# Kernel tuning notes

Hardware: AMD Instinct MI355X
Metric: run time of the kernel (lower is better)

## Reference

```python
import jax, jax.numpy as jnp
from jax import lax
import numpy as np

B, C, T = 8, 1024, 4096
H, K = 16, 7
PAD_L, PAD_R = 6, 0  # causal padding = kernel_size - 1
STRIDE = 1


def setup_inputs() -> dict:
    key = jax.random.key(0)
    k1, k2 = jax.random.split(key)
    x = jax.random.normal(k1, (B, C, T), dtype=jnp.float32)
    # xavier_uniform for [H, 1, K]: bound = sqrt(6 / (fan_in + fan_out)) with fan_in=K, fan_out=H*K? torch uses fan_in=1*K, fan_out=H*K/ groups... use simple uniform scale ~ sqrt(6/(1*K + 1*K))
    bound = float(np.sqrt(6.0 / (K + K)))
    weight = jax.random.uniform(k2, (H, 1, K), dtype=jnp.float32, minval=-bound, maxval=bound)
    bias = jnp.zeros((H,), dtype=jnp.float32)
    return {"x": x, "weight": weight, "bias": bias}


def reference(x, weight, bias):
    """Lightweight convolution: softmax-normalized shared-weight depthwise conv1d.
    x: [B, C, T]; weight: [H, 1, K]; bias: [H].
    """
    b, c, t = x.shape
    h = weight.shape[0]
    n = c // h  # channels per head sharing one kernel
    w = jax.nn.softmax(weight, axis=-1)  # [H, 1, K]
    # fold the shared-channel groups into the batch dim: [B*N, H, T]
    xr = x.reshape(b * n, h, t)
    xp = jnp.pad(xr, ((0, 0), (0, 0), (PAD_L, PAD_R)))
    out = lax.conv_general_dilated(
        xp, w,
        window_strides=(STRIDE,),
        padding='VALID',
        dimension_numbers=('NCH', 'OIH', 'NCH'),
        feature_group_count=h,
    )  # [B*N, H, T]
    out = out + bias[None, :, None]
    return out.reshape(b, c, t)
```

## Files before the change

kernel.cpp:

```cpp
#include <hip/hip_runtime.h>
#include <math.h>

#define TT 4096
#define KK 7
#define HH 16

__global__ void softmax_w_kernel(const float* __restrict__ w,
                                 float* __restrict__ wsm) {
    int h = threadIdx.x;
    if (h < HH) {
        float v[KK];
        float m = -1e30f;
        #pragma unroll
        for (int k = 0; k < KK; ++k) { v[k] = w[h * KK + k]; m = fmaxf(m, v[k]); }
        float s = 0.f;
        #pragma unroll
        for (int k = 0; k < KK; ++k) { v[k] = expf(v[k] - m); s += v[k]; }
        float inv = 1.f / s;
        #pragma unroll
        for (int k = 0; k < KK; ++k) wsm[h * KK + k] = v[k] * inv;
    }
}

__global__ __launch_bounds__(256) void lightconv_kernel(
    const float* __restrict__ x, const float* __restrict__ wsm,
    const float* __restrict__ bias, float* __restrict__ out) {
    const int Q   = blockIdx.x * 256 + threadIdx.x;
    const int row = Q >> 10;
    const int tq  = Q & 1023;
    const int h   = row & (HH - 1);

    const float w0 = wsm[h * KK + 0], w1 = wsm[h * KK + 1], w2 = wsm[h * KK + 2],
                w3 = wsm[h * KK + 3], w4 = wsm[h * KK + 4], w5 = wsm[h * KK + 5],
                w6 = wsm[h * KK + 6];
    const float bb = bias[h];

    const float4* xr = (const float4*)(x + (size_t)row * TT);
    float4 q2 = xr[tq];
    float4 q1 = make_float4(0.f, 0.f, 0.f, 0.f);
    float4 q0 = make_float4(0.f, 0.f, 0.f, 0.f);
    if (tq >= 1) q1 = xr[tq - 1];
    if (tq >= 2) q0 = xr[tq - 2];

    float f[12] = {q0.x, q0.y, q0.z, q0.w,
                   q1.x, q1.y, q1.z, q1.w,
                   q2.x, q2.y, q2.z, q2.w};

    float4 o;
    float* op = &o.x;
    #pragma unroll
    for (int j = 0; j < 4; ++j) {
        float acc = bb;
        acc = fmaf(w0, f[j + 2], acc);
        acc = fmaf(w1, f[j + 3], acc);
        acc = fmaf(w2, f[j + 4], acc);
        acc = fmaf(w3, f[j + 5], acc);
        acc = fmaf(w4, f[j + 6], acc);
        acc = fmaf(w5, f[j + 7], acc);
        acc = fmaf(w6, f[j + 8], acc);
        op[j] = acc;
    }
    ((float4*)(out + (size_t)row * TT))[tq] = o;
}

extern "C" void kernel_launch(void* const* d_in, const int* in_sizes, int n_in,
                              void* d_out, int out_size, void* d_ws, size_t ws_size,
                              hipStream_t stream) {
    const float* x    = (const float*)d_in[0];
    const float* w    = (const float*)d_in[1];
    const float* bias = (const float*)d_in[2];
    float* out = (float*)d_out;
    float* wsm = (float*)d_ws;

    softmax_w_kernel<<<1, 64, 0, stream>>>(w, wsm);

    const int totalQ = out_size / 4;
    lightconv_kernel<<<totalQ / 256, 256, 0, stream>>>(x, wsm, bias, out);
}
```

Before: 228.1 us.

## Fuse softmax into conv kernel and stage each row in shared memory

Drops the separate softmax launch: every block now recomputes the softmax of its head's 7 weights in registers. Each block handles a whole row of 4096 samples and loads it once into LDS, so the overlapping neighbour reads come from shared memory instead of three global float4 loads per thread. This saves one launch and redundant global reads, at the cost of a __syncthreads, 16KB of LDS per block and fewer, larger blocks.

```diff
diff --git a/kernel.cpp b/kernel.cpp
--- a/kernel.cpp
+++ b/kernel.cpp
@@ -5,62 +5,54 @@
 #define KK 7
 #define HH 16
 
-__global__ void softmax_w_kernel(const float* __restrict__ w,
-                                 float* __restrict__ wsm) {
-    int h = threadIdx.x;
-    if (h < HH) {
-        float v[KK];
-        float m = -1e30f;
-        #pragma unroll
-        for (int k = 0; k < KK; ++k) { v[k] = w[h * KK + k]; m = fmaxf(m, v[k]); }
-        float s = 0.f;
-        #pragma unroll
-        for (int k = 0; k < KK; ++k) { v[k] = expf(v[k] - m); s += v[k]; }
-        float inv = 1.f / s;
-        #pragma unroll
-        for (int k = 0; k < KK; ++k) wsm[h * KK + k] = v[k] * inv;
-    }
-}
-
 __global__ __launch_bounds__(256) void lightconv_kernel(
-    const float* __restrict__ x, const float* __restrict__ wsm,
+    const float* __restrict__ x, const float* __restrict__ w,
     const float* __restrict__ bias, float* __restrict__ out) {
-    const int Q   = blockIdx.x * 256 + threadIdx.x;
-    const int row = Q >> 10;
-    const int tq  = Q & 1023;
+    const int row = blockIdx.x;
     const int h   = row & (HH - 1);
 
-    const float w0 = wsm[h * KK + 0], w1 = wsm[h * KK + 1], w2 = wsm[h * KK + 2],
-                w3 = wsm[h * KK + 3], w4 = wsm[h * KK + 4], w5 = wsm[h * KK + 5],
-                w6 = wsm[h * KK + 6];
+    float wk[KK];
+    #pragma unroll
+    for (int k = 0; k < KK; ++k) wk[k] = w[h * KK + k];
+    float m = wk[0];
+    #pragma unroll
+    for (int k = 1; k < KK; ++k) m = fmaxf(m, wk[k]);
+    float s = 0.f;
+    #pragma unroll
+    for (int k = 0; k < KK; ++k) { wk[k] = __expf(wk[k] - m); s += wk[k]; }
+    const float inv = 1.f / s;
+    #pragma unroll
+    for (int k = 0; k < KK; ++k) wk[k] *= inv;
     const float bb = bias[h];
 
+    __shared__ float4 sv[2 + TT / 4];
     const float4* xr = (const float4*)(x + (size_t)row * TT);
-    float4 q2 = xr[tq];
-    float4 q1 = make_float4(0.f, 0.f, 0.f, 0.f);
-    float4 q0 = make_float4(0.f, 0.f, 0.f, 0.f);
-    if (tq >= 1) q1 = xr[tq - 1];
-    if (tq >= 2) q0 = xr[tq - 2];
+    const int tid = threadIdx.x;
+    if (tid < 2) sv[tid] = make_float4(0.f, 0.f, 0.f, 0.f);
+    #pragma unroll
+    for (int n = 0; n < 4; ++n) sv[2 + n * 256 + tid] = xr[n * 256 + tid];
+    __syncthreads();
 
-    float f[12] = {q0.x, q0.y, q0.z, q0.w,
-                   q1.x, q1.y, q1.z, q1.w,
-                   q2.x, q2.y, q2.z, q2.w};
-
-    float4 o;
-    float* op = &o.x;
+    float4* outr = (float4*)(out + (size_t)row * TT);
     #pragma unroll
-    for (int j = 0; j < 4; ++j) {
-        float acc = bb;
-        acc = fmaf(w0, f[j + 2], acc);
-        acc = fmaf(w1, f[j + 3], acc);
-        acc = fmaf(w2, f[j + 4], acc);
-        acc = fmaf(w3, f[j + 5], acc);
-        acc = fmaf(w4, f[j + 6], acc);
-        acc = fmaf(w5, f[j + 7], acc);
-        acc = fmaf(w6, f[j + 8], acc);
-        op[j] = acc;
+    for (int n = 0; n < 4; ++n) {
+        const int q = n * 256 + tid;
+        float4 a = sv[q];
+        float4 b = sv[q + 1];
+        float4 c = sv[q + 2];
+        float f[12] = {a.x, a.y, a.z, a.w, b.x, b.y, b.z, b.w,
+                       c.x, c.y, c.z, c.w};
+        float4 o;
+        float* op = &o.x;
+        #pragma unroll
+        for (int j = 0; j < 4; ++j) {
+            float acc = bb;
+            #pragma unroll
+            for (int k = 0; k < KK; ++k) acc = fmaf(wk[k], f[j + k + 2], acc);
+            op[j] = acc;
+        }
+        outr[q] = o;
     }
-    ((float4*)(out + (size_t)row * TT))[tq] = o;
 }
 
 extern "C" void kernel_launch(void* const* d_in, const int* in_sizes, int n_in,
@@ -70,10 +62,7 @@
     const float* w    = (const float*)d_in[1];
     const float* bias = (const float*)d_in[2];
     float* out = (float*)d_out;
-    float* wsm = (float*)d_ws;
 
-    softmax_w_kernel<<<1, 64, 0, stream>>>(w, wsm);
-
-    const int totalQ = out_size / 4;
-    lightconv_kernel<<<totalQ / 256, 256, 0, stream>>>(x, wsm, bias, out);
+    const int rows = out_size / TT;
+    lightconv_kernel<<<rows, 256, 0, stream>>>(x, w, bias, out);
 }
```

New measurement: 230.5 us. Within noise of the previous version (+1.0%).
